# Kernel tuning notes

Hardware: AMD Instinct MI355X
Metric: run time of the kernel (lower is better)

Reference implementation:

```python
import jax, jax.numpy as jnp
import numpy as np

N_POINTS = 131072
N_SEG = 16
C = 256
BN_EPS = 1e-5


def setup_inputs() -> dict:
    key = jax.random.key(0)
    ks = jax.random.split(key, 6)
    x = jax.random.normal(ks[0], (N_POINTS, C), jnp.float32)
    # Ragged segment end-offsets (cumulative counts), strictly increasing, last == N_POINTS.
    rng = np.random.default_rng(0)
    base = N_POINTS // N_SEG
    counts = base + rng.integers(-base // 32, base // 32, N_SEG)
    counts[-1] += N_POINTS - counts.sum()
    o = jnp.asarray(np.cumsum(counts), jnp.int32)
    s1 = 1.0 / np.sqrt(2 * C)  # linear1: Linear(2C -> C)
    s2 = 1.0 / np.sqrt(C)      # linear2: Linear(C -> C)
    W1 = jax.random.uniform(ks[1], (2 * C, C), jnp.float32, -s1, s1)
    b1 = jax.random.uniform(ks[2], (C,), jnp.float32, -s1, s1)
    W2 = jax.random.uniform(ks[3], (C, C), jnp.float32, -s2, s2)
    b2 = jax.random.uniform(ks[4], (C,), jnp.float32, -s2, s2)
    gamma = jnp.ones((C,), jnp.float32)
    beta = jnp.zeros((C,), jnp.float32)
    return {"x": x, "o": o, "W1": W1, "b1": b1, "W2": W2, "b2": b2,
            "gamma": gamma, "beta": beta}


def reference(x, o, W1, b1, W2, b2, gamma, beta):
    n, c = x.shape
    s = o.shape[0]
    # segment id per point from cumulative end-offsets
    seg_id = jnp.searchsorted(o, jnp.arange(n), side="right")  # [N]
    counts = jnp.concatenate([o[:1], o[1:] - o[:-1]])          # [S]
    # per-segment mean pooling (x_b.sum(0, True) / cnt)
    sums = jax.ops.segment_sum(x, seg_id, num_segments=s)      # [S, C]
    means = sums / counts[:, None].astype(x.dtype)
    # linear2: Linear(C, C) + ReLU on segment means
    y = jax.nn.relu(means @ W2 + b2)                           # [S, C]
    # broadcast-concat back to points, then linear1: Linear(2C, C)
    h = jnp.concatenate([x, y[seg_id]], axis=1) @ W1 + b1      # [N, C]
    # BatchNorm1d (training mode: batch statistics, biased variance) + ReLU
    mu = h.mean(axis=0)
    var = h.var(axis=0)
    out = jax.nn.relu((h - mu) * (gamma / jnp.sqrt(var + BN_EPS)) + beta)
    return out
```

## Files before the change

kernel.cpp:

```cpp
#include <hip/hip_runtime.h>
#include <stdint.h>

#define N_PTS 131072
#define NC 256
#define NSEG 16
#define BN_EPSF 1e-5f

typedef __attribute__((ext_vector_type(8))) short bf16x8;
typedef __attribute__((ext_vector_type(4))) float f32x4;

__device__ __forceinline__ unsigned short f2bf(float f) {
  union { float f; uint32_t u; } v; v.f = f;
  uint32_t u = v.u;
  uint32_t r = (u + 0x7fffu + ((u >> 16) & 1u)) >> 16;
  return (unsigned short)r;
}
__device__ __forceinline__ float bf2f(unsigned short h) {
  union { uint32_t u; float f; } v; v.u = ((uint32_t)h) << 16; return v.f;
}

__device__ __forceinline__ int swz(int col, int row) {
  return (col & ~63) | ((((col >> 3) & 7) ^ (row & 7)) << 3) | (col & 7);
}

__device__ __forceinline__ void gll16(const unsigned short* g, unsigned short* l) {
  __builtin_amdgcn_global_load_lds(
      (const __attribute__((address_space(1))) void*)g,
      (__attribute__((address_space(3))) void*)l, 16, 0, 0);
}

__global__ __launch_bounds__(256) void k_prep(const float* __restrict__ W1,
                                              unsigned short* __restrict__ w1t,
                                              float* __restrict__ zerobuf) {
  int b = blockIdx.x, t = threadIdx.x;
  if (b >= 16) {
    int i = (b - 16) * 256 + t;
    if (i < 8448) zerobuf[i] = 0.f;
    return;
  }
  __shared__ float tile[64][65];
  int bx = b & 3, by = b >> 2;
  int k0 = by * 64, j0 = bx * 64;
  int r = t >> 6, c = t & 63;
#pragma unroll
  for (int i = 0; i < 16; ++i) {
    int kk = r + i * 4;
    tile[kk][c] = W1[(size_t)(k0 + kk) * NC + j0 + c];
  }
  __syncthreads();
#pragma unroll
  for (int i = 0; i < 16; ++i) {
    int jj = r + i * 4;
    int row = j0 + jj, col = k0 + c;
    w1t[(size_t)row * NC + swz(col, row)] = f2bf(tile[c][jj]);
  }
}

__global__ __launch_bounds__(512, 4) void k_gemm1(
    const float* __restrict__ x, const int* __restrict__ o,
    const unsigned short* __restrict__ w1t,
    unsigned short* __restrict__ g_bf,
    float* __restrict__ seg_sums, float* __restrict__ hseg,
    float* __restrict__ gsumsq) {
  __shared__ __align__(16) unsigned short lA[64 * NC];
  __shared__ __align__(16) unsigned short lB[NC * 64];
  __shared__ float s_acc[2][NC];
  __shared__ float s_hA[NC], s_hB[NC], s_q[NC];
  __shared__ int o_s[NSEG];
  int t = threadIdx.x, lane = t & 63, w = t >> 6;
  int row0 = blockIdx.x * 64;
  if (t < NSEG) o_s[t] = o[t];
  if (t < NC) { s_acc[0][t] = 0.f; s_acc[1][t] = 0.f; }
  __syncthreads();

#pragma unroll
  for (int i = 0; i < 4; ++i) {
    int tp = t + i * 512;
    gll16(w1t + (size_t)(tp >> 3) * NC + (tp & 7) * 8, lB + tp * 8);
  }

  int c0 = lane * 4;
  int s0 = 0;
  while (o_s[s0] <= row0) ++s0;
  int e0 = o_s[s0];
  int s1 = (s0 < NSEG - 1) ? s0 + 1 : s0;

  {
    float4 accA = {0.f, 0.f, 0.f, 0.f}, accB = {0.f, 0.f, 0.f, 0.f};
    const float4* xv = (const float4*)x;
#pragma unroll
    for (int i = 0; i < 8; ++i) {
      int rl = w + i * 8;
      int r = row0 + rl;
      float4 v = xv[(size_t)r * 64 + lane];
      ushort4 b;
      b.x = f2bf(v.x); b.y = f2bf(v.y); b.z = f2bf(v.z); b.w = f2bf(v.w);
      *(ushort4*)(lA + rl * NC + swz(c0, rl)) = b;
      bool inA = (r < e0);
      accA.x += inA ? v.x : 0.f; accB.x += inA ? 0.f : v.x;
      accA.y += inA ? v.y : 0.f; accB.y += inA ? 0.f : v.y;
      accA.z += inA ? v.z : 0.f; accB.z += inA ? 0.f : v.z;
      accA.w += inA ? v.w : 0.f; accB.w += inA ? 0.f : v.w;
    }
    atomicAdd(&s_acc[0][c0 + 0], accA.x);
    atomicAdd(&s_acc[0][c0 + 1], accA.y);
    atomicAdd(&s_acc[0][c0 + 2], accA.z);
    atomicAdd(&s_acc[0][c0 + 3], accA.w);
    atomicAdd(&s_acc[1][c0 + 0], accB.x);
    atomicAdd(&s_acc[1][c0 + 1], accB.y);
    atomicAdd(&s_acc[1][c0 + 2], accB.z);
    atomicAdd(&s_acc[1][c0 + 3], accB.w);
  }

  f32x4 acc[4][2] = {};
  for (int kt = 0; kt < 4; ++kt) {
    if (kt > 0) {
#pragma unroll
      for (int i = 0; i < 4; ++i) {
        int tp = t + i * 512;
        gll16(w1t + (size_t)(tp >> 3) * NC + kt * 64 + (tp & 7) * 8, lB + tp * 8);
      }
    }
    __syncthreads();
#pragma unroll
    for (int kk = 0; kk < 2; ++kk) {
      bf16x8 af[4], bfr[2];
      int sl = kk * 4 + (lane >> 4);
#pragma unroll
      for (int mm = 0; mm < 4; ++mm) {
        int r = mm * 16 + (lane & 15);
        af[mm] = *(const bf16x8*)(lA + r * NC + kt * 64 + ((sl ^ (r & 7)) << 3));
      }
#pragma unroll
      for (int nn = 0; nn < 2; ++nn) {
        int jrow = w * 32 + nn * 16 + (lane & 15);
        bfr[nn] = *(const bf16x8*)(lB + jrow * 64 + ((sl ^ (jrow & 7)) << 3));
      }
#pragma unroll
      for (int mm = 0; mm < 4; ++mm)
#pragma unroll
        for (int nn = 0; nn < 2; ++nn)
          acc[mm][nn] = __builtin_amdgcn_mfma_f32_16x16x32_bf16(bfr[nn], af[mm],
                                                                acc[mm][nn], 0, 0, 0);
    }
    __syncthreads();
  }

  int rl = lane & 15, q = lane >> 4;
#pragma unroll
  for (int nn = 0; nn < 2; ++nn) {
    float tA[4] = {0.f, 0.f, 0.f, 0.f};
    float tB[4] = {0.f, 0.f, 0.f, 0.f};
    float tq[4] = {0.f, 0.f, 0.f, 0.f};
#pragma unroll
    for (int mm = 0; mm < 4; ++mm) {
      int row = row0 + mm * 16 + rl;
      bool inA = (row < e0);
      ushort4 b;
#pragma unroll
      for (int r = 0; r < 4; ++r) {
        float gv = acc[mm][nn][r];
        tA[r] += inA ? gv : 0.f;
        tB[r] += inA ? 0.f : gv;
        tq[r] += gv * gv;
        ((unsigned short*)&b)[r] = f2bf(gv);
      }
      *(ushort4*)(g_bf + (size_t)row * NC + w * 32 + nn * 16 + q * 4) = b;
    }
#pragma unroll
    for (int r = 0; r < 4; ++r) {
      tA[r] += __shfl_xor(tA[r], 1, 64); tA[r] += __shfl_xor(tA[r], 2, 64);
      tA[r] += __shfl_xor(tA[r], 4, 64); tA[r] += __shfl_xor(tA[r], 8, 64);
      tB[r] += __shfl_xor(tB[r], 1, 64); tB[r] += __shfl_xor(tB[r], 2, 64);
      tB[r] += __shfl_xor(tB[r], 4, 64); tB[r] += __shfl_xor(tB[r], 8, 64);
      tq[r] += __shfl_xor(tq[r], 1, 64); tq[r] += __shfl_xor(tq[r], 2, 64);
      tq[r] += __shfl_xor(tq[r], 4, 64); tq[r] += __shfl_xor(tq[r], 8, 64);
    }
    if (rl == 0) {
#pragma unroll
      for (int r = 0; r < 4; ++r) {
        int col = w * 32 + nn * 16 + q * 4 + r;
        s_hA[col] = tA[r]; s_hB[col] = tB[r]; s_q[col] = tq[r];
      }
    }
  }
  __syncthreads();
  if (t < NC) {
    atomicAdd(&seg_sums[s0 * NC + t], s_acc[0][t]);
    atomicAdd(&seg_sums[s1 * NC + t], s_acc[1][t]);
    atomicAdd(&hseg[s0 * NC + t], s_hA[t]);
    atomicAdd(&hseg[s1 * NC + t], s_hB[t]);
    atomicAdd(&gsumsq[t], s_q[t]);
  }
}

__global__ __launch_bounds__(256) void k_seg_mlp(
    const int* __restrict__ o, const float* __restrict__ seg_sums,
    const float* __restrict__ W1, const float* __restrict__ b1,
    const float* __restrict__ W2, const float* __restrict__ b2,
    float* __restrict__ z) {
  __shared__ float mean_s[NC];
  __shared__ float y_s[NC];
  int b = blockIdx.x, j = threadIdx.x;
  int start = (b == 0) ? 0 : o[b - 1];
  float inv = 1.f / (float)(o[b] - start);
  mean_s[j] = seg_sums[b * NC + j] * inv;
  __syncthreads();
  float a = b2[j];
  for (int k = 0; k < NC; ++k) a += mean_s[k] * W2[k * NC + j];
  y_s[j] = fmaxf(a, 0.f);
  __syncthreads();
  float a2 = b1[j];
  for (int k = 0; k < NC; ++k) a2 += y_s[k] * W1[(NC + k) * NC + j];
  z[b * NC + j] = a2;
}

__global__ __launch_bounds__(256) void k_apply(
    const unsigned short* __restrict__ g_bf, const int* __restrict__ o,
    const float* __restrict__ z, const float* __restrict__ hseg,
    const float* __restrict__ gsumsq, const float* __restrict__ gamma,
    const float* __restrict__ beta, float* __restrict__ out) {
  __shared__ float s_scale[NC], s_shift[NC];
  __shared__ int o_s[NSEG];
  int t = threadIdx.x;
  int row0 = blockIdx.x * 64;
  if (t < NSEG) o_s[t] = o[t];
  __syncthreads();
  {
    float cs = 0.f, cq = gsumsq[t];
    int prev = 0;
#pragma unroll
    for (int s = 0; s < NSEG; ++s) {
      float cnt = (float)(o_s[s] - prev);
      prev = o_s[s];
      float hs = hseg[s * NC + t], zz = z[s * NC + t];
      cs += hs + cnt * zz;
      cq += (2.f * hs + cnt * zz) * zz;
    }
    float invN = 1.f / (float)N_PTS;
    float mu = cs * invN;
    float var = cq * invN - mu * mu;
    float sc = gamma[t] * rsqrtf(var + BN_EPSF);
    s_scale[t] = sc;
    s_shift[t] = beta[t] - mu * sc;
  }
  __syncthreads();
  int s0 = 0;
  while (o_s[s0] <= row0) ++s0;
  int e0 = o_s[s0];
  int s1 = (s0 < NSEG - 1) ? s0 + 1 : s0;
  int cg = (t & 31) * 8, rsub = t >> 5;
  float4 sc0 = *(const float4*)(s_scale + cg), sc1 = *(const float4*)(s_scale + cg + 4);
  float4 sh0 = *(const float4*)(s_shift + cg), sh1 = *(const float4*)(s_shift + cg + 4);
  float4 zA0 = *(const float4*)(z + s0 * NC + cg), zA1 = *(const float4*)(z + s0 * NC + cg + 4);
  float4 zB0 = *(const float4*)(z + s1 * NC + cg), zB1 = *(const float4*)(z + s1 * NC + cg + 4);
#pragma unroll
  for (int i = 0; i < 8; ++i) {
    int row = row0 + rsub + i * 8;
    uint4 hv = *(const uint4*)(g_bf + (size_t)row * NC + cg);
    bool inA = (row < e0);
    float4 z0 = inA ? zA0 : zB0;
    float4 z1 = inA ? zA1 : zB1;
    float4 o0, o1;
    o0.x = fmaxf((bf2f((unsigned short)(hv.x & 0xffffu)) + z0.x) * sc0.x + sh0.x, 0.f);
    o0.y = fmaxf((bf2f((unsigned short)(hv.x >> 16)) + z0.y) * sc0.y + sh0.y, 0.f);
    o0.z = fmaxf((bf2f((unsigned short)(hv.y & 0xffffu)) + z0.z) * sc0.z + sh0.z, 0.f);
    o0.w = fmaxf((bf2f((unsigned short)(hv.y >> 16)) + z0.w) * sc0.w + sh0.w, 0.f);
    o1.x = fmaxf((bf2f((unsigned short)(hv.z & 0xffffu)) + z1.x) * sc1.x + sh1.x, 0.f);
    o1.y = fmaxf((bf2f((unsigned short)(hv.z >> 16)) + z1.y) * sc1.y + sh1.y, 0.f);
    o1.z = fmaxf((bf2f((unsigned short)(hv.w & 0xffffu)) + z1.z) * sc1.z + sh1.z, 0.f);
    o1.w = fmaxf((bf2f((unsigned short)(hv.w >> 16)) + z1.w) * sc1.w + sh1.w, 0.f);
    *(float4*)(out + (size_t)row * NC + cg) = o0;
    *(float4*)(out + (size_t)row * NC + cg + 4) = o1;
  }
}

extern "C" void kernel_launch(void* const* d_in, const int* in_sizes, int n_in,
                              void* d_out, int out_size, void* d_ws, size_t ws_size,
                              hipStream_t stream) {
  const float* x = (const float*)d_in[0];
  const int* o = (const int*)d_in[1];
  const float* W1 = (const float*)d_in[2];
  const float* b1 = (const float*)d_in[3];
  const float* W2 = (const float*)d_in[4];
  const float* b2 = (const float*)d_in[5];
  const float* gamma = (const float*)d_in[6];
  const float* beta = (const float*)d_in[7];
  float* out = (float*)d_out;

  char* ws = (char*)d_ws;
  unsigned short* g_bf = (unsigned short*)ws;
  char* base2 = ws + 67108864;
  float* seg_sums = (float*)(base2);
  float* hseg     = (float*)(base2 + 16384);
  float* gsumsq   = (float*)(base2 + 32768);
  float* z        = (float*)(base2 + 33792);
  unsigned short* w1t = (unsigned short*)(base2 + 50176);

  k_prep<<<49, 256, 0, stream>>>(W1, w1t, seg_sums);
  k_gemm1<<<2048, 512, 0, stream>>>(x, o, w1t, g_bf, seg_sums, hseg, gsumsq);
  k_seg_mlp<<<16, 256, 0, stream>>>(o, seg_sums, W1, b1, W2, b2, z);
  k_apply<<<2048, 256, 0, stream>>>(g_bf, o, z, hseg, gsumsq, gamma, beta, out);
}
```

Before: 346.4 us.

## Make gemm1 persistent over four row tiles with register-resident W1 fragments

Each k_gemm1 block now handles 256 rows as four 64-row tiles instead of one, with a quarter as many blocks. W1 fragments are loaded once into registers and kept there, not streamed through LDS for every tile. The next tile's x rows are prefetched into registers while the current tile is computed, using a double-buffered A tile in LDS. Segment and statistic partial sums are carried across tiles so there are fewer global atomics. The cost is higher register pressure (launch bounds drop to 2 blocks per CU) and less parallelism, with 512 blocks on a 256-CU part. One segment boundary per 256 rows is assumed; with segments of roughly 8K rows, that assumption holds for these inputs.

Result: faster. 311.6 us (-10.0%).

```diff
diff --git a/kernel.cpp b/kernel.cpp
--- a/kernel.cpp
+++ b/kernel.cpp
@@ -21,12 +21,6 @@
 
 __device__ __forceinline__ int swz(int col, int row) {
   return (col & ~63) | ((((col >> 3) & 7) ^ (row & 7)) << 3) | (col & 7);
-}
-
-__device__ __forceinline__ void gll16(const unsigned short* g, unsigned short* l) {
-  __builtin_amdgcn_global_load_lds(
-      (const __attribute__((address_space(1))) void*)g,
-      (__attribute__((address_space(3))) void*)l, 16, 0, 0);
 }
 
 __global__ __launch_bounds__(256) void k_prep(const float* __restrict__ W1,
@@ -51,146 +45,156 @@
 #pragma unroll
   for (int i = 0; i < 16; ++i) {
     int jj = r + i * 4;
-    int row = j0 + jj, col = k0 + c;
-    w1t[(size_t)row * NC + swz(col, row)] = f2bf(tile[c][jj]);
-  }
-}
-
-__global__ __launch_bounds__(512, 4) void k_gemm1(
+    w1t[(size_t)(j0 + jj) * NC + k0 + c] = f2bf(tile[c][jj]);
+  }
+}
+
+__global__ __launch_bounds__(512, 2) void k_gemm1(
     const float* __restrict__ x, const int* __restrict__ o,
     const unsigned short* __restrict__ w1t,
     unsigned short* __restrict__ g_bf,
     float* __restrict__ seg_sums, float* __restrict__ hseg,
     float* __restrict__ gsumsq) {
-  __shared__ __align__(16) unsigned short lA[64 * NC];
-  __shared__ __align__(16) unsigned short lB[NC * 64];
-  __shared__ float s_acc[2][NC];
-  __shared__ float s_hA[NC], s_hB[NC], s_q[NC];
+  __shared__ __align__(16) unsigned short lA[2][64 * NC];
+  __shared__ float s_xacc[2][NC];
+  __shared__ float s_gA[NC], s_gB[NC], s_gq[NC];
   __shared__ int o_s[NSEG];
   int t = threadIdx.x, lane = t & 63, w = t >> 6;
-  int row0 = blockIdx.x * 64;
+  int rowB = blockIdx.x * 256;
   if (t < NSEG) o_s[t] = o[t];
-  if (t < NC) { s_acc[0][t] = 0.f; s_acc[1][t] = 0.f; }
-  __syncthreads();
-
-#pragma unroll
-  for (int i = 0; i < 4; ++i) {
-    int tp = t + i * 512;
-    gll16(w1t + (size_t)(tp >> 3) * NC + (tp & 7) * 8, lB + tp * 8);
-  }
-
+  if (t < NC) { s_xacc[0][t] = 0.f; s_xacc[1][t] = 0.f; }
+  __syncthreads();
+  int sA = 0;
+  while (o_s[sA] <= rowB) ++sA;
+  int e = o_s[sA];
+  int sB = (sA < NSEG - 1) ? sA + 1 : sA;
+
+  bf16x8 Bf[4][2][2];
+  {
+    int jr0 = w * 32 + (lane & 15);
+    int sl0 = lane >> 4;
+#pragma unroll
+    for (int kt = 0; kt < 4; ++kt)
+#pragma unroll
+      for (int kk = 0; kk < 2; ++kk)
+#pragma unroll
+        for (int nn = 0; nn < 2; ++nn)
+          Bf[kt][kk][nn] = *(const bf16x8*)(
+              w1t + (size_t)(jr0 + nn * 16) * NC + kt * 64 + (kk * 4 + sl0) * 8);
+  }
+
+  float4 xaccA = {0.f, 0.f, 0.f, 0.f}, xaccB = {0.f, 0.f, 0.f, 0.f};
+  f32x4 pA[2] = {}, pB[2] = {}, pq[2] = {};
+  f32x4 acc[4][2] = {};
+  const float4* xv = (const float4*)x;
   int c0 = lane * 4;
-  int s0 = 0;
-  while (o_s[s0] <= row0) ++s0;
-  int e0 = o_s[s0];
-  int s1 = (s0 < NSEG - 1) ? s0 + 1 : s0;
-
-  {
-    float4 accA = {0.f, 0.f, 0.f, 0.f}, accB = {0.f, 0.f, 0.f, 0.f};
-    const float4* xv = (const float4*)x;
+  float4 xr[8];
+#pragma unroll
+  for (int i = 0; i < 8; ++i)
+    xr[i] = xv[(size_t)(rowB + w + i * 8) * 64 + lane];
+
+  for (int tile = 0; tile < 4; ++tile) {
+    int row0 = rowB + tile * 64;
+    int buf = tile & 1;
 #pragma unroll
     for (int i = 0; i < 8; ++i) {
       int rl = w + i * 8;
       int r = row0 + rl;
-      float4 v = xv[(size_t)r * 64 + lane];
+      float4 v = xr[i];
       ushort4 b;
       b.x = f2bf(v.x); b.y = f2bf(v.y); b.z = f2bf(v.z); b.w = f2bf(v.w);
-      *(ushort4*)(lA + rl * NC + swz(c0, rl)) = b;
-      bool inA = (r < e0);
-      accA.x += inA ? v.x : 0.f; accB.x += inA ? 0.f : v.x;
-      accA.y += inA ? v.y : 0.f; accB.y += inA ? 0.f : v.y;
-      accA.z += inA ? v.z : 0.f; accB.z += inA ? 0.f : v.z;
-      accA.w += inA ? v.w : 0.f; accB.w += inA ? 0.f : v.w;
-    }
-    atomicAdd(&s_acc[0][c0 + 0], accA.x);
-    atomicAdd(&s_acc[0][c0 + 1], accA.y);
-    atomicAdd(&s_acc[0][c0 + 2], accA.z);
-    atomicAdd(&s_acc[0][c0 + 3], accA.w);
-    atomicAdd(&s_acc[1][c0 + 0], accB.x);
-    atomicAdd(&s_acc[1][c0 + 1], accB.y);
-    atomicAdd(&s_acc[1][c0 + 2], accB.z);
-    atomicAdd(&s_acc[1][c0 + 3], accB.w);
-  }
-
-  f32x4 acc[4][2] = {};
-  for (int kt = 0; kt < 4; ++kt) {
-    if (kt > 0) {
-#pragma unroll
-      for (int i = 0; i < 4; ++i) {
-        int tp = t + i * 512;
-        gll16(w1t + (size_t)(tp >> 3) * NC + kt * 64 + (tp & 7) * 8, lB + tp * 8);
+      *(ushort4*)(&lA[buf][rl * NC + swz(c0, rl)]) = b;
+      bool inA = (r < e);
+      xaccA.x += inA ? v.x : 0.f; xaccB.x += inA ? 0.f : v.x;
+      xaccA.y += inA ? v.y : 0.f; xaccB.y += inA ? 0.f : v.y;
+      xaccA.z += inA ? v.z : 0.f; xaccB.z += inA ? 0.f : v.z;
+      xaccA.w += inA ? v.w : 0.f; xaccB.w += inA ? 0.f : v.w;
+    }
+    if (tile < 3) {
+#pragma unroll
+      for (int i = 0; i < 8; ++i)
+        xr[i] = xv[(size_t)(row0 + 64 + w + i * 8) * 64 + lane];
+    }
+    __syncthreads();
+
+#pragma unroll
+    for (int kt = 0; kt < 4; ++kt)
+#pragma unroll
+      for (int kk = 0; kk < 2; ++kk) {
+        bf16x8 af[4];
+        int sl = kk * 4 + (lane >> 4);
+#pragma unroll
+        for (int mm = 0; mm < 4; ++mm) {
+          int r = mm * 16 + (lane & 15);
+          af[mm] = *(const bf16x8*)(&lA[buf][r * NC + kt * 64 + ((sl ^ (r & 7)) << 3)]);
+        }
+#pragma unroll
+        for (int mm = 0; mm < 4; ++mm)
+#pragma unroll
+          for (int nn = 0; nn < 2; ++nn)
+            acc[mm][nn] = __builtin_amdgcn_mfma_f32_16x16x32_bf16(
+                Bf[kt][kk][nn], af[mm], acc[mm][nn], 0, 0, 0);
       }
-    }
-    __syncthreads();
-#pragma unroll
-    for (int kk = 0; kk < 2; ++kk) {
-      bf16x8 af[4], bfr[2];
-      int sl = kk * 4 + (lane >> 4);
-#pragma unroll
-      for (int mm = 0; mm < 4; ++mm) {
-        int r = mm * 16 + (lane & 15);
-        af[mm] = *(const bf16x8*)(lA + r * NC + kt * 64 + ((sl ^ (r & 7)) << 3));
-      }
-#pragma unroll
-      for (int nn = 0; nn < 2; ++nn) {
-        int jrow = w * 32 + nn * 16 + (lane & 15);
-        bfr[nn] = *(const bf16x8*)(lB + jrow * 64 + ((sl ^ (jrow & 7)) << 3));
-      }
-#pragma unroll
-      for (int mm = 0; mm < 4; ++mm)
-#pragma unroll
-        for (int nn = 0; nn < 2; ++nn)
-          acc[mm][nn] = __builtin_amdgcn_mfma_f32_16x16x32_bf16(bfr[nn], af[mm],
-                                                                acc[mm][nn], 0, 0, 0);
-    }
-    __syncthreads();
-  }
-
-  int rl = lane & 15, q = lane >> 4;
-#pragma unroll
-  for (int nn = 0; nn < 2; ++nn) {
-    float tA[4] = {0.f, 0.f, 0.f, 0.f};
-    float tB[4] = {0.f, 0.f, 0.f, 0.f};
-    float tq[4] = {0.f, 0.f, 0.f, 0.f};
+
+    int rl = lane & 15, q = lane >> 4;
 #pragma unroll
     for (int mm = 0; mm < 4; ++mm) {
       int row = row0 + mm * 16 + rl;
-      bool inA = (row < e0);
-      ushort4 b;
-#pragma unroll
-      for (int r = 0; r < 4; ++r) {
-        float gv = acc[mm][nn][r];
-        tA[r] += inA ? gv : 0.f;
-        tB[r] += inA ? 0.f : gv;
-        tq[r] += gv * gv;
-        ((unsigned short*)&b)[r] = f2bf(gv);
+      bool inA = (row < e);
+#pragma unroll
+      for (int nn = 0; nn < 2; ++nn) {
+        f32x4 g = acc[mm][nn];
+        ushort4 b;
+        b.x = f2bf(g[0]); b.y = f2bf(g[1]); b.z = f2bf(g[2]); b.w = f2bf(g[3]);
+        *(ushort4*)(g_bf + (size_t)row * NC + w * 32 + nn * 16 + q * 4) = b;
+        if (inA) pA[nn] += g; else pB[nn] += g;
+        pq[nn] += g * g;
+        acc[mm][nn] = (f32x4){0.f, 0.f, 0.f, 0.f};
       }
-      *(ushort4*)(g_bf + (size_t)row * NC + w * 32 + nn * 16 + q * 4) = b;
-    }
-#pragma unroll
-    for (int r = 0; r < 4; ++r) {
-      tA[r] += __shfl_xor(tA[r], 1, 64); tA[r] += __shfl_xor(tA[r], 2, 64);
-      tA[r] += __shfl_xor(tA[r], 4, 64); tA[r] += __shfl_xor(tA[r], 8, 64);
-      tB[r] += __shfl_xor(tB[r], 1, 64); tB[r] += __shfl_xor(tB[r], 2, 64);
-      tB[r] += __shfl_xor(tB[r], 4, 64); tB[r] += __shfl_xor(tB[r], 8, 64);
-      tq[r] += __shfl_xor(tq[r], 1, 64); tq[r] += __shfl_xor(tq[r], 2, 64);
-      tq[r] += __shfl_xor(tq[r], 4, 64); tq[r] += __shfl_xor(tq[r], 8, 64);
-    }
-    if (rl == 0) {
-#pragma unroll
-      for (int r = 0; r < 4; ++r) {
-        int col = w * 32 + nn * 16 + q * 4 + r;
-        s_hA[col] = tA[r]; s_hB[col] = tB[r]; s_q[col] = tq[r];
+    }
+  }
+
+  atomicAdd(&s_xacc[0][c0 + 0], xaccA.x);
+  atomicAdd(&s_xacc[0][c0 + 1], xaccA.y);
+  atomicAdd(&s_xacc[0][c0 + 2], xaccA.z);
+  atomicAdd(&s_xacc[0][c0 + 3], xaccA.w);
+  atomicAdd(&s_xacc[1][c0 + 0], xaccB.x);
+  atomicAdd(&s_xacc[1][c0 + 1], xaccB.y);
+  atomicAdd(&s_xacc[1][c0 + 2], xaccB.z);
+  atomicAdd(&s_xacc[1][c0 + 3], xaccB.w);
+#pragma unroll
+  for (int nn = 0; nn < 2; ++nn)
+#pragma unroll
+    for (int j = 0; j < 4; ++j) {
+      float a = pA[nn][j], bb = pB[nn][j], qq = pq[nn][j];
+      a += __shfl_xor(a, 1, 64); a += __shfl_xor(a, 2, 64);
+      a += __shfl_xor(a, 4, 64); a += __shfl_xor(a, 8, 64);
+      bb += __shfl_xor(bb, 1, 64); bb += __shfl_xor(bb, 2, 64);
+      bb += __shfl_xor(bb, 4, 64); bb += __shfl_xor(bb, 8, 64);
+      qq += __shfl_xor(qq, 1, 64); qq += __shfl_xor(qq, 2, 64);
+      qq += __shfl_xor(qq, 4, 64); qq += __shfl_xor(qq, 8, 64);
+      pA[nn][j] = a; pB[nn][j] = bb; pq[nn][j] = qq;
+    }
+  if ((lane & 15) == 0) {
+    int q = lane >> 4;
+#pragma unroll
+    for (int nn = 0; nn < 2; ++nn) {
+      int cb = w * 32 + nn * 16 + q * 4;
+#pragma unroll
+      for (int j = 0; j < 4; ++j) {
+        s_gA[cb + j] = pA[nn][j];
+        s_gB[cb + j] = pB[nn][j];
+        s_gq[cb + j] = pq[nn][j];
       }
     }
   }
   __syncthreads();
   if (t < NC) {
-    atomicAdd(&seg_sums[s0 * NC + t], s_acc[0][t]);
-    atomicAdd(&seg_sums[s1 * NC + t], s_acc[1][t]);
-    atomicAdd(&hseg[s0 * NC + t], s_hA[t]);
-    atomicAdd(&hseg[s1 * NC + t], s_hB[t]);
-    atomicAdd(&gsumsq[t], s_q[t]);
+    atomicAdd(&seg_sums[sA * NC + t], s_xacc[0][t]);
+    atomicAdd(&seg_sums[sB * NC + t], s_xacc[1][t]);
+    atomicAdd(&hseg[sA * NC + t], s_gA[t]);
+    atomicAdd(&hseg[sB * NC + t], s_gB[t]);
+    atomicAdd(&gsumsq[t], s_gq[t]);
   }
 }
 
@@ -298,7 +302,7 @@
   unsigned short* w1t = (unsigned short*)(base2 + 50176);
 
   k_prep<<<49, 256, 0, stream>>>(W1, w1t, seg_sums);
-  k_gemm1<<<2048, 512, 0, stream>>>(x, o, w1t, g_bf, seg_sums, hseg, gsumsq);
+  k_gemm1<<<512, 512, 0, stream>>>(x, o, w1t, g_bf, seg_sums, hseg, gsumsq);
   k_seg_mlp<<<16, 256, 0, stream>>>(o, seg_sums, W1, b1, W2, b2, z);
   k_apply<<<2048, 256, 0, stream>>>(g_bf, o, z, hseg, gsumsq, gamma, beta, out);
 }
```
